# Optimization experiments

Hardware: AMD Instinct MI355X
Metric: run time of the kernel (lower is better)

The kernel has to match this reference:

```python
import jax, jax.numpy as jnp
import numpy as np

N, B, S, A, H, E = 8, 8192, 64, 16, 512, 4  # agents, batch, state, action, hidden, heads
D = H // E  # attend_dim


def setup_inputs() -> dict:
    key = jax.random.key(0)
    ks = jax.random.split(key, 12)
    g = lambda k, shape, fan: (jax.random.normal(k, shape, jnp.float32) / np.float32(np.sqrt(fan)))
    return {
        "states": jax.random.normal(ks[0], (N, B, S), jnp.float32),
        "actions": jax.random.normal(ks[1], (N, B, A), jnp.float32),
        # per-agent state encoder (Linear + LeakyReLU)
        "Ws": g(ks[2], (N, S, H), S), "bs": jnp.zeros((N, H), jnp.float32),
        # per-agent state-action encoder
        "Wsa": g(ks[3], (N, S + A, H), S + A), "bsa": jnp.zeros((N, H), jnp.float32),
        # shared per-head extractors (key/selector bias-free, value has bias+LeakyReLU)
        "Wk": g(ks[4], (E, H, D), H),
        "Wsel": g(ks[5], (E, H, D), H),
        "Wv": g(ks[6], (E, H, D), H), "bv": jnp.zeros((E, D), jnp.float32),
        # per-agent critic head (2H -> H -> 1)
        "Wc1": g(ks[7], (N, 2 * H, H), 2 * H), "bc1": jnp.zeros((N, H), jnp.float32),
        "Wc2": g(ks[8], (N, H, 1), H), "bc2": jnp.zeros((N, 1), jnp.float32),
        # per-agent value head (2H -> H -> 1)
        "Wv1": g(ks[9], (N, 2 * H, H), 2 * H), "bv1": jnp.zeros((N, H), jnp.float32),
        "Wv2": g(ks[10], (N, H, 1), H), "bv2": jnp.zeros((N, 1), jnp.float32),
    }


def reference(states, actions, Ws, bs, Wsa, bsa, Wk, Wsel, Wv, bv,
              Wc1, bc1, Wc2, bc2, Wv1, bv1, Wv2, bv2):
    lrelu = jax.nn.leaky_relu  # slope 0.01, matches nn.LeakyReLU default
    # encoders: [N,B,H]
    s_enc = lrelu(jnp.einsum('nbs,nsh->nbh', states, Ws) + bs[:, None, :])
    sa = jnp.concatenate([states, actions], axis=-1)
    sa_enc = lrelu(jnp.einsum('nbi,nih->nbh', sa, Wsa) + bsa[:, None, :])
    # per-head keys/selectors/values: [B,E,N,D]
    keys = jnp.einsum('nbh,ehd->bend', sa_enc, Wk)
    sels = jnp.einsum('nbh,ehd->bend', sa_enc, Wsel)
    vals = lrelu(jnp.einsum('nbh,ehd->bend', sa_enc, Wv) + bv[None, :, None, :])
    # each agent i attends over all agents j (including itself; no mask in source)
    logits = jnp.einsum('beid,bejd->beij', sels, keys) / jnp.float32(np.sqrt(D))
    weights = jax.nn.softmax(logits, axis=-1)
    other = jnp.einsum('beij,bejd->beid', weights, vals)  # [B,E,N,D]
    other = jnp.transpose(other, (2, 0, 1, 3)).reshape(N, B, H)  # heads concat -> [N,B,H]
    critic_in = jnp.concatenate([sa_enc, other], axis=-1)  # [N,B,2H]
    value_in = jnp.concatenate([s_enc, other], axis=-1)
    q = jnp.einsum('nbh,nho->nbo', lrelu(jnp.einsum('nbi,nih->nbh', critic_in, Wc1) + bc1[:, None, :]), Wc2) + bc2[:, None, :]
    v = jnp.einsum('nbh,nho->nbo', lrelu(jnp.einsum('nbi,nih->nbh', value_in, Wv1) + bv1[:, None, :]), Wv2) + bv2[:, None, :]
    return q, v  # each [N,B,1]
```

## Files before the change

### kernel.cpp

```cpp
#include <hip/hip_runtime.h>


#define DEVI __device__ __forceinline__

typedef unsigned short us16;
typedef __bf16 bf16x8 __attribute__((ext_vector_type(8)));
typedef float f32x4 __attribute__((ext_vector_type(4)));
typedef unsigned short u16x8 __attribute__((ext_vector_type(8)));

DEVI us16 f2bf(float f) {
  unsigned u = __builtin_bit_cast(unsigned, f);
  u += 0x7FFFu + ((u >> 16) & 1u);
  return (us16)(u >> 16);
}
DEVI float bf2f(us16 h) {
  unsigned u = ((unsigned)h) << 16;
  return __builtin_bit_cast(float, u);
}
DEVI float lrelu(float v) { return v > 0.f ? v : 0.01f * v; }
DEVI int pk2(float a, float b) { return (int)f2bf(a) | ((int)f2bf(b) << 16); }

DEVI void gload16(const us16* g, us16* l) {
  __builtin_amdgcn_global_load_lds(
      (const __attribute__((address_space(1))) void*)g,
      (__attribute__((address_space(3))) void*)l, 16, 0, 0);
}

__global__ void tconv_k(const float* __restrict__ src, long srcSlice, int K, int O,
                        us16* __restrict__ dst, long dstSlice, int dstRowOff,
                        int ldd, int Kpad)
{
  __shared__ float t[32][33];
  const int s = blockIdx.z;
  const int k0 = blockIdx.x * 32, o0 = blockIdx.y * 32;
  const int lx = threadIdx.x, ly = threadIdx.y;
#pragma unroll
  for (int i = 0; i < 4; i++) {
    int k = k0 + ly + i * 8, o = o0 + lx;
    float v = 0.f;
    if (k < K && o < O) v = src[(long)s * srcSlice + (long)k * O + o];
    t[ly + i * 8][lx] = v;
  }
  __syncthreads();
#pragma unroll
  for (int i = 0; i < 4; i++) {
    int o = o0 + ly + i * 8, k = k0 + lx;
    if (o < O && k < Kpad)
      dst[(long)s * dstSlice + (long)(dstRowOff + o) * ldd + k] = f2bf(t[lx][ly + i * 8]);
  }
}

__global__ void tconv3_k(const float* __restrict__ wk, const float* __restrict__ wsel,
                         const float* __restrict__ wv, us16* __restrict__ dst)
{
  __shared__ float t[32][33];
  const int zz = blockIdx.z;
  const int e = zz & 3, m = zz >> 2;
  const float* src = ((m == 0) ? wk : (m == 1) ? wsel : wv) + (long)e * 512 * 128;
  us16* d = dst + (long)e * 384 * 512 + (long)(m * 128) * 512;
  const int k0 = blockIdx.x * 32, o0 = blockIdx.y * 32;
  const int lx = threadIdx.x, ly = threadIdx.y;
#pragma unroll
  for (int i = 0; i < 4; i++)
    t[ly + i * 8][lx] = src[(long)(k0 + ly + i * 8) * 128 + (o0 + lx)];
  __syncthreads();
#pragma unroll
  for (int i = 0; i < 4; i++)
    d[(long)(o0 + ly + i * 8) * 512 + (k0 + lx)] = f2bf(t[lx][ly + i * 8]);
}

__global__ void tconvC_k(const float* __restrict__ c1, const float* __restrict__ v1,
                         us16* __restrict__ dc, us16* __restrict__ dv)
{
  __shared__ float t[32][33];
  const int zz = blockIdx.z;
  const int n = zz & 7, m = zz >> 3;
  const float* src = ((m == 0) ? c1 : v1) + (long)n * 1024 * 512;
  us16* dst = ((m == 0) ? dc : dv) + (long)n * 512 * 1024;
  const int k0 = blockIdx.x * 32, o0 = blockIdx.y * 32;
  const int lx = threadIdx.x, ly = threadIdx.y;
#pragma unroll
  for (int i = 0; i < 4; i++)
    t[ly + i * 8][lx] = src[(long)(k0 + ly + i * 8) * 512 + (o0 + lx)];
  __syncthreads();
#pragma unroll
  for (int i = 0; i < 4; i++)
    dst[(long)(o0 + ly + i * 8) * 1024 + (k0 + lx)] = f2bf(t[lx][ly + i * 8]);
}

enum { ASRC_F32 = 2, ASRC_F32_CAT = 3 };

template <int ASRC, int KTOT>
__global__ __launch_bounds__(256, 4)
void enc_gemm_k(const float* __restrict__ Ap, long aSlice,
                const float* __restrict__ A2p, long a2Slice,
                const us16* __restrict__ Btp, long bSlice,
                const float* __restrict__ bias, long biasSlice,
                us16* __restrict__ outB, long outSlice, long outRow)
{
  __shared__ us16 lA[128 * 32];
  __shared__ us16 lB[128 * 32];
  const int tid = threadIdx.x;
  const int z = blockIdx.z;
  const int m0 = blockIdx.x * 128;
  const int n0 = blockIdx.y * 128;
  const int wv = tid >> 6, lane = tid & 63;
  const int wm = (wv >> 1) * 64, wn = (wv & 1) * 64;
  const int fr = lane & 15, fk = (lane >> 4) * 8;
  const int rbase = (lane >> 4) * 4;
  const int grow = tid >> 2, gcol = (tid & 3) * 8;

  f32x4 acc[4][4];
#pragma unroll
  for (int i = 0; i < 4; i++)
#pragma unroll
    for (int j = 0; j < 4; j++) acc[i][j] = f32x4{0.f, 0.f, 0.f, 0.f};

  const us16* bbase = Btp + (long)z * bSlice + (long)n0 * KTOT;

  for (int k0 = 0; k0 < KTOT; k0 += 32) {
    int4 ra0, ra1;
    {
      const int srow = tid >> 1, scol0 = (tid & 1) * 16;
      const int kg = k0 + scol0;
      const float* a = nullptr;
      if constexpr (ASRC == ASRC_F32) {
        a = Ap + (long)z * aSlice + (long)(m0 + srow) * 64 + kg;
      } else {
        if (kg < 64)      a = Ap + (long)z * aSlice + (long)(m0 + srow) * 64 + kg;
        else if (kg < 80) a = A2p + (long)z * a2Slice + (long)(m0 + srow) * 16 + (kg - 64);
      }
      float4 f0, f1, f2, f3;
      if (a) { const float4* ap = (const float4*)a; f0 = ap[0]; f1 = ap[1]; f2 = ap[2]; f3 = ap[3]; }
      else   { f0 = make_float4(0.f, 0.f, 0.f, 0.f); f1 = f0; f2 = f0; f3 = f0; }
      ra0.x = pk2(f0.x, f0.y); ra0.y = pk2(f0.z, f0.w); ra0.z = pk2(f1.x, f1.y); ra0.w = pk2(f1.z, f1.w);
      ra1.x = pk2(f2.x, f2.y); ra1.y = pk2(f2.z, f2.w); ra1.z = pk2(f3.x, f3.y); ra1.w = pk2(f3.z, f3.w);
    }

    __syncthreads();
    {
      const us16* bb = bbase + k0 + gcol;
      gload16(bb + (long)grow * KTOT, &lB[tid * 8]);
      gload16(bb + (long)(64 + grow) * KTOT, &lB[2048 + tid * 8]);
    }
    {
      const int srow = tid >> 1, scol0 = (tid & 1) * 16;
      *(int4*)&lA[srow * 32 + scol0]     = ra0;
      *(int4*)&lA[srow * 32 + scol0 + 8] = ra1;
    }
    __syncthreads();

    bf16x8 af[4], bfg[4];
#pragma unroll
    for (int f = 0; f < 4; f++) af[f]  = *(const bf16x8*)&lA[(wm + f * 16 + fr) * 32 + fk];
#pragma unroll
    for (int f = 0; f < 4; f++) bfg[f] = *(const bf16x8*)&lB[(wn + f * 16 + fr) * 32 + fk];
#pragma unroll
    for (int fm = 0; fm < 4; fm++)
#pragma unroll
      for (int fn = 0; fn < 4; fn++)
        acc[fm][fn] = __builtin_amdgcn_mfma_f32_16x16x32_bf16(af[fm], bfg[fn], acc[fm][fn], 0, 0, 0);
  }

#pragma unroll
  for (int fm = 0; fm < 4; fm++) {
#pragma unroll
    for (int fn = 0; fn < 4; fn++) {
      int col = n0 + wn + fn * 16 + fr;
      float badd = bias[(long)z * biasSlice + col];
      us16* op = outB + (long)z * outSlice + (long)(m0 + wm + fm * 16 + rbase) * outRow + col;
#pragma unroll
      for (int j = 0; j < 4; j++) {
        float v = lrelu(acc[fm][fn][j] + badd);
        op[(long)j * outRow] = f2bf(v);
      }
    }
  }
}

enum { EPI_KSV = 1, EPI_DOT = 2 };

template <bool CAT, int KTOT>
DEVI void stage32(const us16* __restrict__ Ap, long aSlice,
                  const us16* __restrict__ A2p, long a2Slice,
                  const us16* __restrict__ bbase, int z, int m0, int k0,
                  int tid, us16* ldsA, us16* ldsB)
{
#pragma unroll
  for (int i = 0; i < 2; i++) {
    const int c = i * 256 + tid;
    const int r = c >> 2;
    const int col = ((c & 3) ^ ((r >> 1) & 3)) << 3;
    const us16* a;
    if constexpr (!CAT) {
      a = Ap + (long)z * aSlice + (long)(m0 + r) * KTOT + (k0 + col);
    } else {
      const int kg = k0 + col;
      a = (kg < 512) ? Ap  + (long)z * aSlice  + (long)(m0 + r) * 512 + kg
                     : A2p + (long)z * a2Slice + (long)(m0 + r) * 512 + (kg - 512);
    }
    gload16(a, ldsA + c * 8);
  }
#pragma unroll
  for (int i = 0; i < 2; i++) {
    const int c = i * 256 + tid;
    const int r = c >> 2;
    const int col = ((c & 3) ^ ((r >> 1) & 3)) << 3;
    gload16(bbase + (long)r * KTOT + (k0 + col), ldsB + c * 8);
  }
}

template <bool CAT, int EPI, int KTOT>
__global__ __launch_bounds__(256, 4)
void gemm32db_k(const us16* __restrict__ Ap, long aSlice,
                const us16* __restrict__ A2p, long a2Slice,
                const us16* __restrict__ Btp, long bSlice,
                const float* __restrict__ bias,
                us16* __restrict__ outB, long outSlice, long outRow,
                const float* __restrict__ dotW, float* __restrict__ partial)
{
  __shared__ us16 lds[2][2][128 * 32];
  const int tid = threadIdx.x;
  const int z = blockIdx.z;
  const int m0 = blockIdx.x * 128;
  const int n0 = blockIdx.y * 128;
  const int wv = tid >> 6, lane = tid & 63;
  const int wm = (wv >> 1) * 64, wn = (wv & 1) * 64;
  const int fr = lane & 15, fk = (lane >> 4) * 8;
  const int rbase = (lane >> 4) * 4;
  const int xorkey = ((fr >> 1) & 3) << 3;

  f32x4 acc[4][4];
#pragma unroll
  for (int i = 0; i < 4; i++)
#pragma unroll
    for (int j = 0; j < 4; j++) acc[i][j] = f32x4{0.f, 0.f, 0.f, 0.f};

  const us16* bbase = Btp + (long)z * bSlice + (long)n0 * KTOT;

  constexpr int NT = KTOT / 32;
  stage32<CAT, KTOT>(Ap, aSlice, A2p, a2Slice, bbase, z, m0, 0, tid,
                     &lds[0][0][0], &lds[0][1][0]);

#pragma unroll 2
  for (int t = 0; t < NT - 1; ++t) {
    const int d = t & 1;
    stage32<CAT, KTOT>(Ap, aSlice, A2p, a2Slice, bbase, z, m0, (t + 1) * 32,
                       tid, &lds[d ^ 1][0][0], &lds[d ^ 1][1][0]);
    asm volatile("s_waitcnt vmcnt(4)" ::: "memory");
    __builtin_amdgcn_s_barrier();
    __builtin_amdgcn_sched_barrier(0);

    const us16* la = &lds[d][0][0];
    const us16* lb = &lds[d][1][0];
    bf16x8 af[4], bfg[4];
#pragma unroll
    for (int f = 0; f < 4; f++)
      af[f]  = *(const bf16x8*)&la[(wm + f * 16 + fr) * 32 + (fk ^ xorkey)];
#pragma unroll
    for (int f = 0; f < 4; f++)
      bfg[f] = *(const bf16x8*)&lb[(wn + f * 16 + fr) * 32 + (fk ^ xorkey)];
    __builtin_amdgcn_s_setprio(1);
#pragma unroll
    for (int fm = 0; fm < 4; fm++)
#pragma unroll
      for (int fn = 0; fn < 4; fn++)
        acc[fm][fn] = __builtin_amdgcn_mfma_f32_16x16x32_bf16(af[fm], bfg[fn], acc[fm][fn], 0, 0, 0);
    __builtin_amdgcn_s_setprio(0);
    __builtin_amdgcn_s_barrier();
    __builtin_amdgcn_sched_barrier(0);
  }
  {
    asm volatile("s_waitcnt vmcnt(0)" ::: "memory");
    __builtin_amdgcn_s_barrier();
    __builtin_amdgcn_sched_barrier(0);
    const us16* la = &lds[(NT - 1) & 1][0][0];
    const us16* lb = &lds[(NT - 1) & 1][1][0];
    bf16x8 af[4], bfg[4];
#pragma unroll
    for (int f = 0; f < 4; f++)
      af[f]  = *(const bf16x8*)&la[(wm + f * 16 + fr) * 32 + (fk ^ xorkey)];
#pragma unroll
    for (int f = 0; f < 4; f++)
      bfg[f] = *(const bf16x8*)&lb[(wn + f * 16 + fr) * 32 + (fk ^ xorkey)];
#pragma unroll
    for (int fm = 0; fm < 4; fm++)
#pragma unroll
      for (int fn = 0; fn < 4; fn++)
        acc[fm][fn] = __builtin_amdgcn_mfma_f32_16x16x32_bf16(af[fm], bfg[fn], acc[fm][fn], 0, 0, 0);
  }

  if constexpr (EPI == EPI_DOT) {
    const float* bsl = bias + (long)z * 512;
    const float* wsl = dotW + (long)z * 512;
#pragma unroll
    for (int fm = 0; fm < 4; fm++) {
#pragma unroll
      for (int j = 0; j < 4; j++) {
        float p = 0.f;
#pragma unroll
        for (int fn = 0; fn < 4; fn++) {
          int col = n0 + wn + fn * 16 + fr;
          float v = acc[fm][fn][j] + bsl[col];
          v = lrelu(v);
          p += v * wsl[col];
        }
        p += __shfl_xor(p, 1); p += __shfl_xor(p, 2); p += __shfl_xor(p, 4); p += __shfl_xor(p, 8);
        if (fr == 0) {
          long row = (long)z * 8192 + (m0 + wm + fm * 16 + rbase + j);
          partial[row * 8 + blockIdx.y * 2 + (wv & 1)] = p;
        }
      }
    }
  } else {
#pragma unroll
    for (int fm = 0; fm < 4; fm++) {
#pragma unroll
      for (int fn = 0; fn < 4; fn++) {
        int col = n0 + wn + fn * 16 + fr;
        float badd = 0.f; bool act = false;
        if (col >= 256) { badd = bias[col - 256]; act = true; }
        us16* op = outB + (long)z * outSlice + (long)(m0 + wm + fm * 16 + rbase) * outRow + col;
#pragma unroll
        for (int j = 0; j < 4; j++) {
          float v = acc[fm][fn][j] + badd;
          if (act) v = lrelu(v);
          op[(long)j * outRow] = f2bf(v);
        }
      }
    }
  }
}

__global__ __launch_bounds__(256, 2)
void attn_k(const us16* __restrict__ ksv, us16* __restrict__ other, int e)
{
  __shared__ us16 t[4][8 * 392];
  const int wv = threadIdx.x >> 6, lane = threadIdx.x & 63;
  const long b = (long)blockIdx.x * 4 + wv;
  const us16* src = ksv + b * 3072;
#pragma unroll
  for (int i = 0; i < 6; i++) {
    int c = i * 64 + lane;
    int r = c / 48, cc = c - r * 48;
    *(int4*)&t[wv][r * 392 + cc * 8] = *(const int4*)&src[c * 8];
  }
  __syncthreads();
  const int i = lane >> 3, j = lane & 7;
  const us16* selp = &t[wv][i * 392 + 128];
  const us16* keyp = &t[wv][j * 392];
  float acc = 0.f;
#pragma unroll
  for (int d = 0; d < 128; d += 8) {
    u16x8 s8 = *(const u16x8*)&selp[d];
    u16x8 k8 = *(const u16x8*)&keyp[d];
#pragma unroll
    for (int q = 0; q < 8; q++) acc += bf2f(s8[q]) * bf2f(k8[q]);
  }
  acc *= 0.088388347648318447f;
  float mx = acc;
  mx = fmaxf(mx, __shfl_xor(mx, 1)); mx = fmaxf(mx, __shfl_xor(mx, 2)); mx = fmaxf(mx, __shfl_xor(mx, 4));
  float ex = __expf(acc - mx);
  float sm = ex;
  sm += __shfl_xor(sm, 1); sm += __shfl_xor(sm, 2); sm += __shfl_xor(sm, 4);
  float wsm = ex / sm;
  float wj[8];
  const int ibase = lane & 56;
#pragma unroll
  for (int jj = 0; jj < 8; jj++) wj[jj] = __shfl(wsm, ibase + jj);
  const int dbase = (lane & 7) * 16;
  float o[16];
#pragma unroll
  for (int q = 0; q < 16; q++) o[q] = 0.f;
#pragma unroll
  for (int jj = 0; jj < 8; jj++) {
    u16x8 v0 = *(const u16x8*)&t[wv][jj * 392 + 256 + dbase];
    u16x8 v1 = *(const u16x8*)&t[wv][jj * 392 + 256 + dbase + 8];
    float wgt = wj[jj];
#pragma unroll
    for (int q = 0; q < 8; q++) { o[q] += wgt * bf2f(v0[q]); o[8 + q] += wgt * bf2f(v1[q]); }
  }
  u16x8 r0, r1;
#pragma unroll
  for (int q = 0; q < 8; q++) { r0[q] = f2bf(o[q]); r1[q] = f2bf(o[8 + q]); }
  us16* dst = other + ((long)i * 8192 + b) * 512 + e * 128 + dbase;
  *(u16x8*)&dst[0] = r0;
  *(u16x8*)&dst[8] = r1;
}

__global__ void reduce_dot_k(const float* __restrict__ part, const float* __restrict__ b2,
                             float* __restrict__ out)
{
  int r = blockIdx.x * 256 + threadIdx.x;
  const float4* p = (const float4*)(part + (long)r * 8);
  float4 a = p[0], b = p[1];
  out[r] = b2[r >> 13] + ((a.x + a.y) + (a.z + a.w)) + ((b.x + b.y) + (b.z + b.w));
}

extern "C" void kernel_launch(void* const* d_in, const int* in_sizes, int n_in,
                              void* d_out, int out_size, void* d_ws, size_t ws_size,
                              hipStream_t stream)
{
  const float* states = (const float*)d_in[0];
  const float* actions= (const float*)d_in[1];
  const float* Ws  = (const float*)d_in[2];
  const float* bs  = (const float*)d_in[3];
  const float* Wsa = (const float*)d_in[4];
  const float* bsa = (const float*)d_in[5];
  const float* Wk  = (const float*)d_in[6];
  const float* Wsel= (const float*)d_in[7];
  const float* Wv  = (const float*)d_in[8];
  const float* bv  = (const float*)d_in[9];
  const float* Wc1 = (const float*)d_in[10];
  const float* bc1 = (const float*)d_in[11];
  const float* Wc2 = (const float*)d_in[12];
  const float* bc2 = (const float*)d_in[13];
  const float* Wv1 = (const float*)d_in[14];
  const float* bv1 = (const float*)d_in[15];
  const float* Wv2 = (const float*)d_in[16];
  const float* bv2 = (const float*)d_in[17];

  char* ws = (char*)d_ws;
  constexpr size_t OFF_WST   = 0;
  constexpr size_t OFF_WSAT  = OFF_WST   + (size_t)8 * 512 * 64 * 2;
  constexpr size_t OFF_WKVST = OFF_WSAT  + (size_t)8 * 512 * 96 * 2;
  constexpr size_t OFF_WC1T  = OFF_WKVST + (size_t)4 * 384 * 512 * 2;
  constexpr size_t OFF_WV1T  = OFF_WC1T  + (size_t)8 * 512 * 1024 * 2;
  constexpr size_t OFF_ENC   = OFF_WV1T  + (size_t)8 * 512 * 1024 * 2;
  constexpr size_t OFF_OTHER = OFF_ENC   + (size_t)8 * 8192 * 512 * 2;
  constexpr size_t OFF_KSV   = OFF_OTHER + (size_t)8 * 8192 * 512 * 2;
  constexpr size_t OFF_PART  = OFF_KSV   + (size_t)8192 * 8 * 384 * 2;
  constexpr size_t NEED      = OFF_PART  + (size_t)65536 * 8 * 4;
  if (ws_size < NEED) return;

  us16* WST   = (us16*)(ws + OFF_WST);
  us16* WSAT  = (us16*)(ws + OFF_WSAT);
  us16* WKVST = (us16*)(ws + OFF_WKVST);
  us16* WC1T  = (us16*)(ws + OFF_WC1T);
  us16* WV1T  = (us16*)(ws + OFF_WV1T);
  us16* ENC   = (us16*)(ws + OFF_ENC);
  us16* OTHER = (us16*)(ws + OFF_OTHER);
  us16* KSV   = (us16*)(ws + OFF_KSV);
  float* PART = (float*)(ws + OFF_PART);

  dim3 tb(32, 8);
  tconv_k <<<dim3(2, 16, 8),  tb, 0, stream>>>(Ws,  (long)64 * 512, 64, 512, WST,  (long)512 * 64, 0, 64, 64);
  tconv_k <<<dim3(3, 16, 8),  tb, 0, stream>>>(Wsa, (long)80 * 512, 80, 512, WSAT, (long)512 * 96, 0, 96, 96);
  tconv3_k<<<dim3(16, 4, 12), tb, 0, stream>>>(Wk, Wsel, Wv, WKVST);
  tconvC_k<<<dim3(32, 16, 16),tb, 0, stream>>>(Wc1, Wv1, WC1T, WV1T);

  enc_gemm_k<ASRC_F32_CAT, 96><<<dim3(64, 4, 8), 256, 0, stream>>>(
      states, (long)8192 * 64, actions, (long)8192 * 16, WSAT, (long)512 * 96, bsa, 512,
      ENC, (long)8192 * 512, 512);

  for (int e = 0; e < 4; e++) {
    gemm32db_k<false, EPI_KSV, 512><<<dim3(64, 3, 8), 256, 0, stream>>>(
        ENC, (long)8192 * 512, nullptr, 0, WKVST + (size_t)e * 384 * 512, 0, bv + e * 128,
        KSV, 384, 3072, nullptr, nullptr);
    attn_k<<<dim3(2048), 256, 0, stream>>>(KSV, OTHER, e);
  }

  gemm32db_k<true, EPI_DOT, 1024><<<dim3(64, 4, 8), 256, 0, stream>>>(
      ENC, (long)8192 * 512, OTHER, (long)8192 * 512, WC1T, (long)512 * 1024, bc1,
      nullptr, 0, 0, Wc2, PART);
  reduce_dot_k<<<dim3(256), 256, 0, stream>>>(PART, bc2, (float*)d_out);

  enc_gemm_k<ASRC_F32, 64><<<dim3(64, 4, 8), 256, 0, stream>>>(
      states, (long)8192 * 64, nullptr, 0, WST, (long)512 * 64, bs, 512,
      ENC, (long)8192 * 512, 512);

  gemm32db_k<true, EPI_DOT, 1024><<<dim3(64, 4, 8), 256, 0, stream>>>(
      ENC, (long)8192 * 512, OTHER, (long)8192 * 512, WV1T, (long)512 * 1024, bv1,
      nullptr, 0, 0, Wv2, PART);
  reduce_dot_k<<<dim3(256), 256, 0, stream>>>(PART, bv2, (float*)d_out + 65536);
}
```

Measured before the change: 445.1 us.

## Add 256x256-tile pipelined GEMM for critic/value heads, single-buffer BK64 elsewhere

Adds a 512-thread GEMM kernel with 256x256 output tiles, 64-wide K steps, 128KB dynamic LDS double buffering, and staged prefetch interleaved with MFMA phases. It is used for the two large concatenated-input critic/value GEMMs with the fused bias/LeakyReLU/dot epilogue. The goal is more operand reuse per byte loaded and fewer blocks. The older double-buffered BK32 kernel is replaced by a simpler single-buffered BK64 kernel for the KSV GEMMs and as a fallback. That kernel synchronises on every K step and does not overlap loads with compute. The big tile runs at low occupancy and depends on the dynamic shared-memory attribute call succeeding.

```diff
diff --git a/kernel.cpp b/kernel.cpp
--- a/kernel.cpp
+++ b/kernel.cpp
@@ -180,46 +180,17 @@
 
 enum { EPI_KSV = 1, EPI_DOT = 2 };
 
-template <bool CAT, int KTOT>
-DEVI void stage32(const us16* __restrict__ Ap, long aSlice,
-                  const us16* __restrict__ A2p, long a2Slice,
-                  const us16* __restrict__ bbase, int z, int m0, int k0,
-                  int tid, us16* ldsA, us16* ldsB)
-{
-#pragma unroll
-  for (int i = 0; i < 2; i++) {
-    const int c = i * 256 + tid;
-    const int r = c >> 2;
-    const int col = ((c & 3) ^ ((r >> 1) & 3)) << 3;
-    const us16* a;
-    if constexpr (!CAT) {
-      a = Ap + (long)z * aSlice + (long)(m0 + r) * KTOT + (k0 + col);
-    } else {
-      const int kg = k0 + col;
-      a = (kg < 512) ? Ap  + (long)z * aSlice  + (long)(m0 + r) * 512 + kg
-                     : A2p + (long)z * a2Slice + (long)(m0 + r) * 512 + (kg - 512);
-    }
-    gload16(a, ldsA + c * 8);
-  }
-#pragma unroll
-  for (int i = 0; i < 2; i++) {
-    const int c = i * 256 + tid;
-    const int r = c >> 2;
-    const int col = ((c & 3) ^ ((r >> 1) & 3)) << 3;
-    gload16(bbase + (long)r * KTOT + (k0 + col), ldsB + c * 8);
-  }
-}
-
 template <bool CAT, int EPI, int KTOT>
 __global__ __launch_bounds__(256, 4)
-void gemm32db_k(const us16* __restrict__ Ap, long aSlice,
-                const us16* __restrict__ A2p, long a2Slice,
-                const us16* __restrict__ Btp, long bSlice,
-                const float* __restrict__ bias,
-                us16* __restrict__ outB, long outSlice, long outRow,
-                const float* __restrict__ dotW, float* __restrict__ partial)
-{
-  __shared__ us16 lds[2][2][128 * 32];
+void gemm64_k(const us16* __restrict__ Ap, long aSlice,
+              const us16* __restrict__ A2p, long a2Slice,
+              const us16* __restrict__ Btp, long bSlice,
+              const float* __restrict__ bias,
+              us16* __restrict__ outB, long outSlice, long outRow,
+              const float* __restrict__ dotW, float* __restrict__ partial)
+{
+  __shared__ us16 lA[128 * 64];
+  __shared__ us16 lB[128 * 64];
   const int tid = threadIdx.x;
   const int z = blockIdx.z;
   const int m0 = blockIdx.x * 128;
@@ -228,7 +199,7 @@
   const int wm = (wv >> 1) * 64, wn = (wv & 1) * 64;
   const int fr = lane & 15, fk = (lane >> 4) * 8;
   const int rbase = (lane >> 4) * 4;
-  const int xorkey = ((fr >> 1) & 3) << 3;
+  const int xorkey = (fr & 7) << 3;
 
   f32x4 acc[4][4];
 #pragma unroll
@@ -238,56 +209,48 @@
 
   const us16* bbase = Btp + (long)z * bSlice + (long)n0 * KTOT;
 
-  constexpr int NT = KTOT / 32;
-  stage32<CAT, KTOT>(Ap, aSlice, A2p, a2Slice, bbase, z, m0, 0, tid,
-                     &lds[0][0][0], &lds[0][1][0]);
-
-#pragma unroll 2
-  for (int t = 0; t < NT - 1; ++t) {
-    const int d = t & 1;
-    stage32<CAT, KTOT>(Ap, aSlice, A2p, a2Slice, bbase, z, m0, (t + 1) * 32,
-                       tid, &lds[d ^ 1][0][0], &lds[d ^ 1][1][0]);
-    asm volatile("s_waitcnt vmcnt(4)" ::: "memory");
-    __builtin_amdgcn_s_barrier();
-    __builtin_amdgcn_sched_barrier(0);
-
-    const us16* la = &lds[d][0][0];
-    const us16* lb = &lds[d][1][0];
-    bf16x8 af[4], bfg[4];
-#pragma unroll
-    for (int f = 0; f < 4; f++)
-      af[f]  = *(const bf16x8*)&la[(wm + f * 16 + fr) * 32 + (fk ^ xorkey)];
-#pragma unroll
-    for (int f = 0; f < 4; f++)
-      bfg[f] = *(const bf16x8*)&lb[(wn + f * 16 + fr) * 32 + (fk ^ xorkey)];
-    __builtin_amdgcn_s_setprio(1);
-#pragma unroll
-    for (int fm = 0; fm < 4; fm++)
-#pragma unroll
-      for (int fn = 0; fn < 4; fn++)
-        acc[fm][fn] = __builtin_amdgcn_mfma_f32_16x16x32_bf16(af[fm], bfg[fn], acc[fm][fn], 0, 0, 0);
-    __builtin_amdgcn_s_setprio(0);
-    __builtin_amdgcn_s_barrier();
-    __builtin_amdgcn_sched_barrier(0);
-  }
-  {
-    asm volatile("s_waitcnt vmcnt(0)" ::: "memory");
-    __builtin_amdgcn_s_barrier();
-    __builtin_amdgcn_sched_barrier(0);
-    const us16* la = &lds[(NT - 1) & 1][0][0];
-    const us16* lb = &lds[(NT - 1) & 1][1][0];
-    bf16x8 af[4], bfg[4];
-#pragma unroll
-    for (int f = 0; f < 4; f++)
-      af[f]  = *(const bf16x8*)&la[(wm + f * 16 + fr) * 32 + (fk ^ xorkey)];
-#pragma unroll
-    for (int f = 0; f < 4; f++)
-      bfg[f] = *(const bf16x8*)&lb[(wn + f * 16 + fr) * 32 + (fk ^ xorkey)];
-#pragma unroll
-    for (int fm = 0; fm < 4; fm++)
-#pragma unroll
-      for (int fn = 0; fn < 4; fn++)
-        acc[fm][fn] = __builtin_amdgcn_mfma_f32_16x16x32_bf16(af[fm], bfg[fn], acc[fm][fn], 0, 0, 0);
+  for (int k0 = 0; k0 < KTOT; k0 += 64) {
+    __syncthreads();
+#pragma unroll
+    for (int i = 0; i < 4; i++) {
+      const int c = i * 256 + tid;
+      const int r = c >> 3;
+      const int col = ((c & 7) ^ (r & 7)) << 3;
+      const us16* a;
+      if constexpr (!CAT) {
+        a = Ap + (long)z * aSlice + (long)(m0 + r) * KTOT + (k0 + col);
+      } else {
+        const int kg = k0 + col;
+        a = (kg < 512) ? Ap  + (long)z * aSlice  + (long)(m0 + r) * 512 + kg
+                       : A2p + (long)z * a2Slice + (long)(m0 + r) * 512 + (kg - 512);
+      }
+      gload16(a, &lA[c * 8]);
+    }
+#pragma unroll
+    for (int i = 0; i < 4; i++) {
+      const int c = i * 256 + tid;
+      const int r = c >> 3;
+      const int col = ((c & 7) ^ (r & 7)) << 3;
+      gload16(bbase + (long)r * KTOT + (k0 + col), &lB[c * 8]);
+    }
+    __syncthreads();
+
+#pragma unroll
+    for (int ks = 0; ks < 2; ks++) {
+      bf16x8 af[4], bfg[4];
+      const int kc = ks * 32 + fk;
+#pragma unroll
+      for (int f = 0; f < 4; f++)
+        af[f]  = *(const bf16x8*)&lA[(wm + f * 16 + fr) * 64 + (kc ^ xorkey)];
+#pragma unroll
+      for (int f = 0; f < 4; f++)
+        bfg[f] = *(const bf16x8*)&lB[(wn + f * 16 + fr) * 64 + (kc ^ xorkey)];
+#pragma unroll
+      for (int fm = 0; fm < 4; fm++)
+#pragma unroll
+        for (int fn = 0; fn < 4; fn++)
+          acc[fm][fn] = __builtin_amdgcn_mfma_f32_16x16x32_bf16(af[fm], bfg[fn], acc[fm][fn], 0, 0, 0);
+    }
   }
 
   if constexpr (EPI == EPI_DOT) {
@@ -327,6 +290,135 @@
           if (act) v = lrelu(v);
           op[(long)j * outRow] = f2bf(v);
         }
+      }
+    }
+  }
+}
+
+template <bool CAT, int KTOT>
+__global__ __launch_bounds__(512, 2)
+void gemm256_k(const us16* __restrict__ Ap, long aSlice,
+               const us16* __restrict__ A2p, long a2Slice,
+               const us16* __restrict__ Btp, long bSlice,
+               const float* __restrict__ bias,
+               const float* __restrict__ dotW, float* __restrict__ partial)
+{
+  extern __shared__ us16 lds[];
+  const int tid = threadIdx.x;
+  const int z = blockIdx.z;
+  const int m0 = blockIdx.x * 256;
+  const int n0 = blockIdx.y * 256;
+  const int wv = tid >> 6, lane = tid & 63;
+  const int wr = wv >> 2, wc = wv & 3;
+  const int wmBase = wr * 128, wnBase = wc * 64;
+  const int fr = lane & 15, fk = (lane >> 4) * 8;
+  const int rbase = (lane >> 4) * 4;
+
+  const int srow = tid >> 3;
+  const int scol = ((tid & 7) ^ (srow & 7)) << 3;
+
+  f32x4 acc[8][4];
+#pragma unroll
+  for (int i = 0; i < 8; i++)
+#pragma unroll
+    for (int j = 0; j < 4; j++) acc[i][j] = f32x4{0.f, 0.f, 0.f, 0.f};
+
+  const us16* bb = Btp + (long)z * bSlice + (long)n0 * KTOT;
+
+  auto stA = [&](int dbuf, int k0, int g) {
+    const int r = g * 64 + srow;
+    const us16* a;
+    if constexpr (CAT) {
+      a = (k0 < 512) ? Ap  + (long)z * aSlice  + (long)(m0 + r) * 512 + (k0 + scol)
+                     : A2p + (long)z * a2Slice + (long)(m0 + r) * 512 + (k0 - 512 + scol);
+    } else {
+      a = Ap + (long)z * aSlice + (long)(m0 + r) * KTOT + (k0 + scol);
+    }
+    gload16(a, lds + dbuf * 32768 + g * 4096 + tid * 8);
+  };
+  auto stB = [&](int dbuf, int k0, int g) {
+    const int r = g * 64 + srow;
+    gload16(bb + (long)r * KTOT + (k0 + scol), lds + dbuf * 32768 + 16384 + g * 4096 + tid * 8);
+  };
+
+  constexpr int NT = KTOT / 64;
+#pragma unroll
+  for (int g = 0; g < 4; g++) { stA(0, 0, g); stB(0, 0, g); }
+
+#pragma unroll 1
+  for (int t = 0; t < NT; ++t) {
+    const int d = t & 1;
+    const us16* curA = lds + d * 32768;
+    const us16* curB = lds + d * 32768 + 16384;
+    const int kn = (t + 1) * 64;
+    const bool more = (t + 1 < NT);
+
+    if (more) {
+      stA(d ^ 1, kn, 0); stB(d ^ 1, kn, 0);
+      asm volatile("s_waitcnt vmcnt(2)" ::: "memory");
+    } else {
+      asm volatile("s_waitcnt vmcnt(0)" ::: "memory");
+    }
+    __builtin_amdgcn_sched_barrier(0);
+    __builtin_amdgcn_s_barrier();
+    __builtin_amdgcn_sched_barrier(0);
+
+    bf16x8 bfg[4][2];
+#pragma unroll
+    for (int fb = 0; fb < 4; fb++)
+#pragma unroll
+      for (int ks = 0; ks < 2; ks++) {
+        const int row = wnBase + fb * 16 + fr;
+        bfg[fb][ks] = *(const bf16x8*)&curB[row * 64 + ((ks * 32 + fk) ^ ((row & 7) << 3))];
+      }
+
+#pragma unroll
+    for (int p = 0; p < 4; p++) {
+      bf16x8 af[2][2];
+#pragma unroll
+      for (int f = 0; f < 2; f++)
+#pragma unroll
+        for (int ks = 0; ks < 2; ks++) {
+          const int row = wmBase + (2 * p + f) * 16 + fr;
+          af[f][ks] = *(const bf16x8*)&curA[row * 64 + ((ks * 32 + fk) ^ ((row & 7) << 3))];
+        }
+      if (more && p < 3) { stA(d ^ 1, kn, p + 1); stB(d ^ 1, kn, p + 1); }
+      __builtin_amdgcn_sched_barrier(0);
+      __builtin_amdgcn_s_barrier();
+      __builtin_amdgcn_s_setprio(1);
+#pragma unroll
+      for (int f = 0; f < 2; f++)
+#pragma unroll
+        for (int fn = 0; fn < 4; fn++)
+#pragma unroll
+          for (int ks = 0; ks < 2; ks++)
+            acc[2 * p + f][fn] =
+                __builtin_amdgcn_mfma_f32_16x16x32_bf16(af[f][ks], bfg[fn][ks], acc[2 * p + f][fn], 0, 0, 0);
+      __builtin_amdgcn_s_setprio(0);
+      __builtin_amdgcn_sched_barrier(0);
+      __builtin_amdgcn_s_barrier();
+      __builtin_amdgcn_sched_barrier(0);
+    }
+  }
+
+  const float* bsl = bias + (long)z * 512;
+  const float* wsl = dotW + (long)z * 512;
+#pragma unroll
+  for (int fm = 0; fm < 8; fm++) {
+#pragma unroll
+    for (int j = 0; j < 4; j++) {
+      float p = 0.f;
+#pragma unroll
+      for (int fn = 0; fn < 4; fn++) {
+        int col = n0 + wnBase + fn * 16 + fr;
+        float v = acc[fm][fn][j] + bsl[col];
+        v = lrelu(v);
+        p += v * wsl[col];
+      }
+      p += __shfl_xor(p, 1); p += __shfl_xor(p, 2); p += __shfl_xor(p, 4); p += __shfl_xor(p, 8);
+      if (fr == 0) {
+        long row = (long)z * 8192 + (m0 + wmBase + fm * 16 + rbase + j);
+        partial[row * 8 + blockIdx.y * 4 + wc] = p;
       }
     }
   }
@@ -443,6 +535,10 @@
   us16* KSV   = (us16*)(ws + OFF_KSV);
   float* PART = (float*)(ws + OFF_PART);
 
+  const bool big =
+      hipFuncSetAttribute((const void*)gemm256_k<true, 1024>,
+                          hipFuncAttributeMaxDynamicSharedMemorySize, 131072) == hipSuccess;
+
   dim3 tb(32, 8);
   tconv_k <<<dim3(2, 16, 8),  tb, 0, stream>>>(Ws,  (long)64 * 512, 64, 512, WST,  (long)512 * 64, 0, 64, 64);
   tconv_k <<<dim3(3, 16, 8),  tb, 0, stream>>>(Wsa, (long)80 * 512, 80, 512, WSAT, (long)512 * 96, 0, 96, 96);
@@ -454,23 +550,33 @@
       ENC, (long)8192 * 512, 512);
 
   for (int e = 0; e < 4; e++) {
-    gemm32db_k<false, EPI_KSV, 512><<<dim3(64, 3, 8), 256, 0, stream>>>(
+    gemm64_k<false, EPI_KSV, 512><<<dim3(64, 3, 8), 256, 0, stream>>>(
         ENC, (long)8192 * 512, nullptr, 0, WKVST + (size_t)e * 384 * 512, 0, bv + e * 128,
         KSV, 384, 3072, nullptr, nullptr);
     attn_k<<<dim3(2048), 256, 0, stream>>>(KSV, OTHER, e);
   }
 
-  gemm32db_k<true, EPI_DOT, 1024><<<dim3(64, 4, 8), 256, 0, stream>>>(
-      ENC, (long)8192 * 512, OTHER, (long)8192 * 512, WC1T, (long)512 * 1024, bc1,
-      nullptr, 0, 0, Wc2, PART);
+  if (big) {
+    gemm256_k<true, 1024><<<dim3(32, 2, 8), 512, 131072, stream>>>(
+        ENC, (long)8192 * 512, OTHER, (long)8192 * 512, WC1T, (long)512 * 1024, bc1, Wc2, PART);
+  } else {
+    gemm64_k<true, EPI_DOT, 1024><<<dim3(64, 4, 8), 256, 0, stream>>>(
+        ENC, (long)8192 * 512, OTHER, (long)8192 * 512, WC1T, (long)512 * 1024, bc1,
+        nullptr, 0, 0, Wc2, PART);
+  }
   reduce_dot_k<<<dim3(256), 256, 0, stream>>>(PART, bc2, (float*)d_out);
 
   enc_gemm_k<ASRC_F32, 64><<<dim3(64, 4, 8), 256, 0, stream>>>(
       states, (long)8192 * 64, nullptr, 0, WST, (long)512 * 64, bs, 512,
       ENC, (long)8192 * 512, 512);
 
-  gemm32db_k<true, EPI_DOT, 1024><<<dim3(64, 4, 8), 256, 0, stream>>>(
-      ENC, (long)8192 * 512, OTHER, (long)8192 * 512, WV1T, (long)512 * 1024, bv1,
-      nullptr, 0, 0, Wv2, PART);
+  if (big) {
+    gemm256_k<true, 1024><<<dim3(32, 2, 8), 512, 131072, stream>>>(
+        ENC, (long)8192 * 512, OTHER, (long)8192 * 512, WV1T, (long)512 * 1024, bv1, Wv2, PART);
+  } else {
+    gemm64_k<true, EPI_DOT, 1024><<<dim3(64, 4, 8), 256, 0, stream>>>(
+        ENC, (long)8192 * 512, OTHER, (long)8192 * 512, WV1T, (long)512 * 1024, bv1,
+        nullptr, 0, 0, Wv2, PART);
+  }
   reduce_dot_k<<<dim3(256), 256, 0, stream>>>(PART, bv2, (float*)d_out + 65536);
 }
```

Result: no change. 440.7 us (-1.0%).
